# Performance work log

Hardware: AMD Instinct MI355X
Metric: run time of the kernel (lower is better)

## Reference

```python
import jax, jax.numpy as jnp
import numpy as np

N = 100000    # nodes
E = 1600000   # edges (avg degree 16)
IN = 128      # input feature dim
D = 32        # per-head hidden dim
H = 4         # heads for hidden layers
C = 16        # num_classes (final per-head dim)
NEG = 0.2     # leaky_relu negative slope


def setup_inputs() -> dict:
    key = jax.random.key(0)
    ks = jax.random.split(key, 14)
    s = jnp.float32(0.05)
    f32 = jnp.float32
    inp = {
        "inputs": jax.random.normal(ks[0], (N, IN), f32),
        "src": jax.random.randint(ks[1], (E,), 0, N),
        "dst": jax.random.randint(ks[2], (E,), 0, N),
        # layer 0: IN -> (H, D), no residual
        "W0": jax.random.normal(ks[3], (IN, H * D), f32) * s,
        "al0": jax.random.normal(ks[4], (H, D), f32) * s,
        "ar0": jax.random.normal(ks[5], (H, D), f32) * s,
        # layer 1: H*D -> (H, D), identity residual (dims match)
        "W1": jax.random.normal(ks[6], (H * D, H * D), f32) * s,
        "al1": jax.random.normal(ks[7], (H, D), f32) * s,
        "ar1": jax.random.normal(ks[8], (H, D), f32) * s,
        # final layer: H*D -> (1, C), linear residual projection
        "W2": jax.random.normal(ks[9], (H * D, 1 * C), f32) * s,
        "al2": jax.random.normal(ks[10], (1, C), f32) * s,
        "ar2": jax.random.normal(ks[11], (1, C), f32) * s,
        "resW2": jax.random.normal(ks[12], (H * D, 1 * C), f32) * s,
    }
    return inp


def gat_conv(h, W, al, ar, src, dst, n_heads, out_dim, res=None, act=None):
    # h: (N, F_in) -> out: (N, n_heads, out_dim)
    feat = (h @ W).reshape(N, n_heads, out_dim)            # (N,H,D)
    el = jnp.sum(feat * al, axis=-1)                       # (N,H)
    er = jnp.sum(feat * ar, axis=-1)                       # (N,H)
    e = jax.nn.leaky_relu(el[src] + er[dst], NEG)          # (E,H)
    # softmax over incoming edges per destination node
    emax = jax.ops.segment_max(e, dst, num_segments=N)     # (N,H)
    ex = jnp.exp(e - emax[dst])                            # (E,H)
    den = jax.ops.segment_sum(ex, dst, num_segments=N)     # (N,H)
    alpha = ex / den[dst]                                  # (E,H)
    msg = feat[src] * alpha[:, :, None]                    # (E,H,D) -- dominant traffic
    out = jax.ops.segment_sum(msg, dst, num_segments=N)    # (N,H,D)
    if res is not None:
        out = out + res
    if act is not None:
        out = act(out)
    return out


def reference(inputs, src, dst, W0, al0, ar0, W1, al1, ar1, W2, al2, ar2, resW2):
    # hidden layer 0 (no residual), GATConv activation = elu, then flatten + relu
    h = gat_conv(inputs, W0, al0, ar0, src, dst, H, D, res=None, act=jax.nn.elu)
    h = jax.nn.relu(h.reshape(N, H * D))
    # hidden layer 1, identity residual (in == H*D)
    res1 = h.reshape(N, H, D)
    h = gat_conv(h, W1, al1, ar1, src, dst, H, D, res=res1, act=jax.nn.elu)
    h = jax.nn.relu(h.reshape(N, H * D))
    # output layer: 1 head, linear residual projection, no activation, mean over heads
    res2 = (h @ resW2).reshape(N, 1, C)
    out = gat_conv(h, W2, al2, ar2, src, dst, 1, C, res=res2, act=None)
    return out.mean(axis=1)                                # (N, C)
```

## Files before the change

### kernel.cpp

```cpp
#include <hip/hip_runtime.h>

#define N_NODES 100000
#define N_EDGES 1600000
#define IN_F    128
#define NEG_SLOPE 0.2f
#define NBUCK   512
#define BCAP    5120
#define PCHUNK  4096
#define PGRID   391
#define GEMMGRID 1563

typedef __attribute__((ext_vector_type(8))) short bf16x8;
typedef __attribute__((ext_vector_type(4))) float f32x4;

__device__ __forceinline__ float bf2f(unsigned short u) {
    return __uint_as_float(((unsigned int)u) << 16);
}

__device__ __forceinline__ unsigned short f2bf(float f) {
    unsigned int u = __float_as_uint(f);
    u += 0x7FFFu + ((u >> 16) & 1u);
    return (unsigned short)(u >> 16);
}

__global__ __launch_bounds__(256) void init_pack(int* __restrict__ bcursor,
                                                 const float* __restrict__ W0,
                                                 const float* __restrict__ W1,
                                                 const float* __restrict__ W2,
                                                 const float* __restrict__ rW2,
                                                 unsigned short* __restrict__ W0p,
                                                 unsigned short* __restrict__ W1p,
                                                 unsigned short* __restrict__ W2p) {
    const int t = threadIdx.x;
    if (blockIdx.x < 2) {
        int i = blockIdx.x * 256 + t;
        if (i < NBUCK) bcursor[i] = i * BCAP;
        return;
    }
    int gid = (blockIdx.x - 2) * 256 + t;
    const float* W;
    unsigned short* Wp;
    int idx, ncols;
    if (gid < 16384)      { W = W0; Wp = W0p; idx = gid;          ncols = 128; }
    else if (gid < 32768) { W = W1; Wp = W1p; idx = gid - 16384;  ncols = 128; }
    else                  { W = W2; Wp = W2p; idx = gid - 32768;  ncols = 32;  }
    int j  = idx & 7;
    int l  = (idx >> 3) & 63;
    int kt = (idx >> 9) & 3;
    int nt = idx >> 11;
    int k  = kt * 32 + (l >> 4) * 8 + j;
    int n  = nt * 16 + (l & 15);
    float v;
    if (ncols == 128) v = W[k * 128 + n];
    else              v = (n < 16) ? W[k * 16 + n] : rW2[k * 16 + (n - 16)];
    Wp[idx] = f2bf(v);
}

__global__ __launch_bounds__(256) void part_gemm0(const int* __restrict__ src,
                                                  const int* __restrict__ dst,
                                                  int* __restrict__ bcursor,
                                                  unsigned int* __restrict__ pe, int nE,
                                                  const float* __restrict__ A,
                                                  const unsigned short* __restrict__ Wp,
                                                  const float* __restrict__ al,
                                                  const float* __restrict__ ar,
                                                  unsigned short* __restrict__ featb,
                                                  float* __restrict__ el,
                                                  float* __restrict__ er,
                                                  int nrows) {
    __shared__ int hist[NBUCK];
    __shared__ int lstart[NBUCK];
    __shared__ int gbase[NBUCK];
    __shared__ int curB[NBUCK];
    __shared__ int s[NBUCK];
    __shared__ unsigned int reorder[PCHUNK];

    const int t = threadIdx.x;

    if (blockIdx.x < PGRID) {
        const int start = blockIdx.x * PCHUNK;

        hist[t] = 0; hist[t + 256] = 0;
        __syncthreads();
#pragma unroll
        for (int j = 0; j < PCHUNK / 256; ++j) {
            int e = start + j * 256 + t;
            if (e < nE) atomicAdd(&hist[dst[e] >> 8], 1);
        }
        __syncthreads();
        const int c0 = hist[t];
        const int c1 = hist[t + 256];
        s[t] = c0; s[t + 256] = c1;
        __syncthreads();
#pragma unroll
        for (int off = 1; off <= 256; off <<= 1) {
            int x0 = (t >= off) ? s[t - off] : 0;
            int x1 = s[t + 256 - off];
            __syncthreads();
            s[t] += x0; s[t + 256] += x1;
            __syncthreads();
        }
        lstart[t]       = s[t] - c0;
        lstart[t + 256] = s[t + 256] - c1;
        curB[t]         = s[t] - c0;
        curB[t + 256]   = s[t + 256] - c1;
        gbase[t]        = c0 ? atomicAdd(&bcursor[t],       c0) : 0;
        gbase[t + 256]  = c1 ? atomicAdd(&bcursor[t + 256], c1) : 0;
        __syncthreads();

#pragma unroll
        for (int j = 0; j < PCHUNK / 256; ++j) {
            int e = start + j * 256 + t;
            if (e < nE) {
                int d  = dst[e];
                int sv = src[e];
                int b  = d >> 8;
                int pos = atomicAdd(&curB[b], 1);
                reorder[pos] = ((unsigned)sv << 8) | ((unsigned)d & 255u);
            }
        }
        __syncthreads();

        for (int b = t; b < NBUCK; b += 256) {
            int st = lstart[b];
            int en = curB[b];
            int gb = gbase[b];
            for (int k = st; k < en; ++k)
                pe[gb + (k - st)] = reorder[k];
        }
    } else {
        const int bid  = blockIdx.x - PGRID;
        const int wv   = t >> 6;
        const int lane = t & 63;
        const int q    = lane >> 4;
        const int m    = lane & 15;
        const int rb   = bid * 64 + wv * 16;
        const int arow = rb + m;
        const bool rok = arow < nrows;
        const float* Ar = A + (size_t)arow * IN_F;

        f32x4 acc[8];
#pragma unroll
        for (int nt = 0; nt < 8; ++nt) acc[nt] = (f32x4){0.f, 0.f, 0.f, 0.f};

#pragma unroll
        for (int kt = 0; kt < 4; ++kt) {
            bf16x8 afr = (bf16x8){0, 0, 0, 0, 0, 0, 0, 0};
            if (rok) {
                float4 v0 = *(const float4*)(Ar + kt * 32 + q * 8);
                float4 v1 = *(const float4*)(Ar + kt * 32 + q * 8 + 4);
                afr[0] = (short)f2bf(v0.x); afr[1] = (short)f2bf(v0.y);
                afr[2] = (short)f2bf(v0.z); afr[3] = (short)f2bf(v0.w);
                afr[4] = (short)f2bf(v1.x); afr[5] = (short)f2bf(v1.y);
                afr[6] = (short)f2bf(v1.z); afr[7] = (short)f2bf(v1.w);
            }
#pragma unroll
            for (int nt = 0; nt < 8; ++nt) {
                bf16x8 bfr = *(const bf16x8*)(Wp + ((size_t)(nt * 4 + kt) * 64 + lane) * 8);
                acc[nt] = __builtin_amdgcn_mfma_f32_16x16x32_bf16(afr, bfr, acc[nt], 0, 0, 0);
            }
        }

        float pel[16], per[16];
#pragma unroll
        for (int i = 0; i < 16; ++i) { pel[i] = 0.f; per[i] = 0.f; }

#pragma unroll
        for (int nt = 0; nt < 8; ++nt) {
            const int col = nt * 16 + m;
            const float alv = al[col];
            const float arv = ar[col];
            const int h = nt >> 1;
#pragma unroll
            for (int reg = 0; reg < 4; ++reg) {
                int row = rb + q * 4 + reg;
                float a = acc[nt][reg];
                if (row < nrows) featb[(size_t)row * 128 + col] = f2bf(a);
                pel[reg * 4 + h] += a * alv;
                per[reg * 4 + h] += a * arv;
            }
        }
#pragma unroll
        for (int sh = 8; sh > 0; sh >>= 1) {
#pragma unroll
            for (int i = 0; i < 16; ++i) {
                pel[i] += __shfl_down(pel[i], sh);
                per[i] += __shfl_down(per[i], sh);
            }
        }
        if (m == 0) {
#pragma unroll
            for (int reg = 0; reg < 4; ++reg) {
                int row = rb + q * 4 + reg;
                if (row < nrows) {
#pragma unroll
                    for (int h = 0; h < 4; ++h) {
                        el[row * 4 + h] = pel[reg * 4 + h];
                        er[row * 4 + h] = per[reg * 4 + h];
                    }
                }
            }
        }
    }
}

__global__ __launch_bounds__(256) void bucket_finalize(const unsigned int* __restrict__ pe,
                                                       const int* __restrict__ bcursor,
                                                       int* __restrict__ rowptr,
                                                       int* __restrict__ deg,
                                                       int* __restrict__ sorted_src) {
    __shared__ int deg_l[256];
    __shared__ int s[256];
    __shared__ int cur[256];

    const int b  = blockIdx.x;
    const int t  = threadIdx.x;
    const int base = b * BCAP;
    const int cnt  = bcursor[b] - base;
    const int n    = b * 256 + t;

    deg_l[t] = 0;
    __syncthreads();
    for (int i = t; i < cnt; i += 256)
        atomicAdd(&deg_l[pe[base + i] & 255u], 1);
    __syncthreads();

    const int dv = deg_l[t];
    s[t] = dv;
    __syncthreads();
#pragma unroll
    for (int off = 1; off < 256; off <<= 1) {
        int x = (t >= off) ? s[t - off] : 0;
        __syncthreads();
        s[t] += x;
        __syncthreads();
    }
    const int off_l = s[t] - dv;
    if (n < N_NODES) {
        rowptr[n] = base + off_l;
        deg[n]    = dv;
    }
    cur[t] = off_l;
    __syncthreads();

    for (int i = t; i < cnt; i += 256) {
        unsigned int ed = pe[base + i];
        int pos = atomicAdd(&cur[ed & 255u], 1);
        sorted_src[base + pos] = (int)(ed >> 8);
    }
}

__global__ __launch_bounds__(256) void gemm128_mfma_bf16(const unsigned short* __restrict__ Ab,
                                                         const unsigned short* __restrict__ Wp,
                                                         const float* __restrict__ al,
                                                         const float* __restrict__ ar,
                                                         unsigned short* __restrict__ featb,
                                                         float* __restrict__ el,
                                                         float* __restrict__ er,
                                                         int nrows) {
    const int t    = threadIdx.x;
    const int wv   = t >> 6;
    const int lane = t & 63;
    const int q    = lane >> 4;
    const int m    = lane & 15;
    const int rb   = blockIdx.x * 64 + wv * 16;
    const int arow = rb + m;
    const bool rok = arow < nrows;
    const unsigned short* Ar = Ab + (size_t)arow * IN_F;

    f32x4 acc[8];
#pragma unroll
    for (int nt = 0; nt < 8; ++nt) acc[nt] = (f32x4){0.f, 0.f, 0.f, 0.f};

#pragma unroll
    for (int kt = 0; kt < 4; ++kt) {
        bf16x8 afr = (bf16x8){0, 0, 0, 0, 0, 0, 0, 0};
        if (rok) afr = *(const bf16x8*)(Ar + kt * 32 + q * 8);
#pragma unroll
        for (int nt = 0; nt < 8; ++nt) {
            bf16x8 bfr = *(const bf16x8*)(Wp + ((size_t)(nt * 4 + kt) * 64 + lane) * 8);
            acc[nt] = __builtin_amdgcn_mfma_f32_16x16x32_bf16(afr, bfr, acc[nt], 0, 0, 0);
        }
    }

    float pel[16], per[16];
#pragma unroll
    for (int i = 0; i < 16; ++i) { pel[i] = 0.f; per[i] = 0.f; }

#pragma unroll
    for (int nt = 0; nt < 8; ++nt) {
        const int col = nt * 16 + m;
        const float alv = al[col];
        const float arv = ar[col];
        const int h = nt >> 1;
#pragma unroll
        for (int reg = 0; reg < 4; ++reg) {
            int row = rb + q * 4 + reg;
            float a = acc[nt][reg];
            if (row < nrows) featb[(size_t)row * 128 + col] = f2bf(a);
            pel[reg * 4 + h] += a * alv;
            per[reg * 4 + h] += a * arv;
        }
    }
#pragma unroll
    for (int sh = 8; sh > 0; sh >>= 1) {
#pragma unroll
        for (int i = 0; i < 16; ++i) {
            pel[i] += __shfl_down(pel[i], sh);
            per[i] += __shfl_down(per[i], sh);
        }
    }
    if (m == 0) {
#pragma unroll
        for (int reg = 0; reg < 4; ++reg) {
            int row = rb + q * 4 + reg;
            if (row < nrows) {
#pragma unroll
                for (int h = 0; h < 4; ++h) {
                    el[row * 4 + h] = pel[reg * 4 + h];
                    er[row * 4 + h] = per[reg * 4 + h];
                }
            }
        }
    }
}

__global__ __launch_bounds__(256) void gemm16_mfma(const unsigned short* __restrict__ Ab,
                                                   const unsigned short* __restrict__ Wp,
                                                   const float* __restrict__ al,
                                                   const float* __restrict__ ar,
                                                   unsigned short* __restrict__ feat2b,
                                                   float* __restrict__ res2,
                                                   float* __restrict__ el,
                                                   float* __restrict__ er,
                                                   int nrows) {
    const int t    = threadIdx.x;
    const int wv   = t >> 6;
    const int lane = t & 63;
    const int q    = lane >> 4;
    const int m    = lane & 15;
    const int rb   = blockIdx.x * 64 + wv * 16;
    const int arow = rb + m;
    const bool rok = arow < nrows;
    const unsigned short* Ar = Ab + (size_t)arow * IN_F;

    f32x4 acc0 = (f32x4){0.f, 0.f, 0.f, 0.f};
    f32x4 acc1 = (f32x4){0.f, 0.f, 0.f, 0.f};

#pragma unroll
    for (int kt = 0; kt < 4; ++kt) {
        bf16x8 afr = (bf16x8){0, 0, 0, 0, 0, 0, 0, 0};
        if (rok) afr = *(const bf16x8*)(Ar + kt * 32 + q * 8);
        bf16x8 b0 = *(const bf16x8*)(Wp + ((size_t)(0 * 4 + kt) * 64 + lane) * 8);
        bf16x8 b1 = *(const bf16x8*)(Wp + ((size_t)(1 * 4 + kt) * 64 + lane) * 8);
        acc0 = __builtin_amdgcn_mfma_f32_16x16x32_bf16(afr, b0, acc0, 0, 0, 0);
        acc1 = __builtin_amdgcn_mfma_f32_16x16x32_bf16(afr, b1, acc1, 0, 0, 0);
    }

    float pel[4], per[4];
    const float alv = al[m];
    const float arv = ar[m];
#pragma unroll
    for (int reg = 0; reg < 4; ++reg) {
        int row = rb + q * 4 + reg;
        float a = acc0[reg];
        if (row < nrows) {
            feat2b[(size_t)row * 16 + m] = f2bf(a);
            res2[(size_t)row * 16 + m]   = acc1[reg];
        }
        pel[reg] = a * alv;
        per[reg] = a * arv;
    }
#pragma unroll
    for (int sh = 8; sh > 0; sh >>= 1) {
#pragma unroll
        for (int reg = 0; reg < 4; ++reg) {
            pel[reg] += __shfl_down(pel[reg], sh);
            per[reg] += __shfl_down(per[reg], sh);
        }
    }
    if (m == 0) {
#pragma unroll
        for (int reg = 0; reg < 4; ++reg) {
            int row = rb + q * 4 + reg;
            if (row < nrows) { el[row] = pel[reg]; er[row] = per[reg]; }
        }
    }
}

#define LOAD16(B, START, CNT)                                                  \
    {                                                                          \
        _Pragma("unroll")                                                      \
        for (int jg_ = 0; jg_ < 16; jg_ += 4) {                                \
            if (jg_ < (CNT)) {                                                 \
                _Pragma("unroll")                                              \
                for (int k_ = 0; k_ < 4; ++k_) {                               \
                    int sj_ = __builtin_amdgcn_readlane(s_own, (START) + jg_ + k_); \
                    const unsigned short* rp_ = featb + (size_t)sj_ * 128;     \
                    (B)[jg_ + k_] = *((const ushort2*)rp_ + lane);             \
                }                                                              \
            }                                                                  \
        }                                                                      \
    }

__global__ __launch_bounds__(256) void gat_agg128(const int* __restrict__ rowptr,
                                                  const int* __restrict__ deg,
                                                  const int* __restrict__ sorted_src,
                                                  const float* __restrict__ el,
                                                  const float* __restrict__ er,
                                                  const unsigned short* __restrict__ featb,
                                                  const unsigned short* __restrict__ resb,
                                                  unsigned short* __restrict__ outb) {
    __shared__ float sW[4][64][4];

    const int wv   = threadIdx.x >> 6;
    const int lane = threadIdx.x & 63;
    const int nd   = blockIdx.x * 4 + wv;

    const int dg = deg[nd];
    const int r0 = rowptr[nd];
    const int h  = lane >> 4;
    const float4 er4 = *(const float4*)(er + nd * 4);

    float den = 0.f;
    float ax = 0.f, ay = 0.f;

    for (int base = 0; base < dg; base += 64) {
        int m = dg - base; if (m > 64) m = 64;

        int s_own = 0;
        if (lane < m) s_own = sorted_src[r0 + base + lane];

        ushort2 u[16], v[16];
        int c = m < 16 ? m : 16;
        LOAD16(u, 0, c)

        float4 w4;
        if (lane < m) {
            float4 e4 = *(const float4*)(el + s_own * 4);
            float t_;
            t_ = e4.x + er4.x; t_ = t_ > 0.f ? t_ : NEG_SLOPE * t_; w4.x = __expf(t_);
            t_ = e4.y + er4.y; t_ = t_ > 0.f ? t_ : NEG_SLOPE * t_; w4.y = __expf(t_);
            t_ = e4.z + er4.z; t_ = t_ > 0.f ? t_ : NEG_SLOPE * t_; w4.z = __expf(t_);
            t_ = e4.w + er4.w; t_ = t_ > 0.f ? t_ : NEG_SLOPE * t_; w4.w = __expf(t_);
        } else {
            w4.x = 0.f; w4.y = 0.f; w4.z = 0.f; w4.w = 0.f;
        }
        *(float4*)(&sW[wv][lane][0]) = w4;

        int i = 0;
        while (true) {
            int in_ = i + c;
            int cn = m - in_; if (cn > 16) cn = 16;
            if (cn > 0) LOAD16(v, in_, cn)

            const float* wb = &sW[wv][i][h];
#pragma unroll
            for (int jg = 0; jg < 16; jg += 4) {
                if (jg < c) {
#pragma unroll
                    for (int k = 0; k < 4; ++k) {
                        float w = wb[(jg + k) * 4];
                        ushort2 uu = u[jg + k];
                        den += w;
                        ax += w * bf2f(uu.x);
                        ay += w * bf2f(uu.y);
                    }
                }
            }
            if (cn <= 0) break;
#pragma unroll
            for (int k = 0; k < 16; ++k) u[k] = v[k];
            i = in_; c = cn;
        }
    }

    float scale = den > 0.f ? 1.f / den : 0.f;
    float ox = ax * scale, oy = ay * scale;
    size_t o0 = (size_t)nd * 128 + lane * 2;
    if (resb) {
        ushort2 rv = *(const ushort2*)(resb + o0);
        ox += bf2f(rv.x);
        oy += bf2f(rv.y);
    }
    ox = fmaxf(ox, 0.f);
    oy = fmaxf(oy, 0.f);
    ushort2 ou;
    ou.x = f2bf(ox);
    ou.y = f2bf(oy);
    *(ushort2*)(outb + o0) = ou;
}

__global__ __launch_bounds__(256) void gat_agg16(const int* __restrict__ rowptr,
                                                 const int* __restrict__ deg,
                                                 const int* __restrict__ sorted_src,
                                                 const float* __restrict__ el,
                                                 const float* __restrict__ er,
                                                 const unsigned short* __restrict__ feat2b,
                                                 const float* __restrict__ res,
                                                 float* __restrict__ out) {
    __shared__ int   sS[4][64];
    __shared__ float sW[4][64];

    const int wv   = threadIdx.x >> 6;
    const int lane = threadIdx.x & 63;
    const int nd   = blockIdx.x * 4 + (threadIdx.x >> 6);
    const int g    = lane >> 3;
    const int f2   = (lane & 7) * 2;

    const int dg = deg[nd];
    const int r0 = rowptr[nd];
    const float erd = er[nd];

    float ax = 0.f, ay = 0.f, den = 0.f;

    for (int base = 0; base < dg; base += 64) {
        int m = dg - base; if (m > 64) m = 64;
        if (lane < m) {
            int s = sorted_src[r0 + base + lane];
            sS[wv][lane] = s;
            float v = el[s] + erd;
            v = v > 0.f ? v : NEG_SLOPE * v;
            sW[wv][lane] = __expf(v);
        }
        for (int i = g; i < m; i += 8) {
            int s   = sS[wv][i];
            float w = sW[wv][i];
            den += w;
            ushort2 u = *(const ushort2*)(feat2b + (size_t)s * 16 + f2);
            ax += w * bf2f(u.x);
            ay += w * bf2f(u.y);
        }
    }

    ax += __shfl_down(ax, 32); ay += __shfl_down(ay, 32); den += __shfl_down(den, 32);
    ax += __shfl_down(ax, 16); ay += __shfl_down(ay, 16); den += __shfl_down(den, 16);
    ax += __shfl_down(ax, 8);  ay += __shfl_down(ay, 8);  den += __shfl_down(den, 8);

    if (lane < 8) {
        float scale = den > 0.f ? 1.f / den : 0.f;
        size_t o0 = (size_t)nd * 16 + f2;
        float2 o;
        o.x = ax * scale + res[o0];
        o.y = ay * scale + res[o0 + 1];
        *(float2*)(out + o0) = o;
    }
}

extern "C" void kernel_launch(void* const* d_in, const int* in_sizes, int n_in,
                              void* d_out, int out_size, void* d_ws, size_t ws_size,
                              hipStream_t stream) {
    const float* inputs = (const float*)d_in[0];
    const int*   src    = (const int*)d_in[1];
    const int*   dst    = (const int*)d_in[2];
    const float* W0     = (const float*)d_in[3];
    const float* al0    = (const float*)d_in[4];
    const float* ar0    = (const float*)d_in[5];
    const float* W1     = (const float*)d_in[6];
    const float* al1    = (const float*)d_in[7];
    const float* ar1    = (const float*)d_in[8];
    const float* W2     = (const float*)d_in[9];
    const float* al2    = (const float*)d_in[10];
    const float* ar2    = (const float*)d_in[11];
    const float* resW2  = (const float*)d_in[12];
    float* out = (float*)d_out;

    const size_t NF = (size_t)N_NODES * 128;
    float* ws   = (float*)d_ws;
    float* el   = ws;
    float* er   = el + (size_t)N_NODES * 4;
    float* res2 = er + (size_t)N_NODES * 4;
    unsigned short* hbufb  = (unsigned short*)(res2 + (size_t)N_NODES * 16);
    unsigned short* featb  = hbufb + NF;
    unsigned short* feat2b = featb + NF;
    unsigned short* W0p    = feat2b + (size_t)N_NODES * 16;
    unsigned short* W1p    = W0p + 16384;
    unsigned short* W2p    = W1p + 16384;
    int* iws = (int*)(W2p + 8192);
    unsigned int* pe = (unsigned int*)iws;
    int* sorted_src  = iws + NBUCK * BCAP;
    int* deg         = sorted_src + NBUCK * BCAP;
    int* rowptr      = deg + N_NODES;
    int* bcursor     = rowptr + N_NODES;

    dim3 blk(256);
    int aggGrid = N_NODES / 4;

    init_pack<<<162, blk, 0, stream>>>(bcursor, W0, W1, W2, resW2, W0p, W1p, W2p);
    part_gemm0<<<PGRID + GEMMGRID, blk, 0, stream>>>(src, dst, bcursor, pe, N_EDGES,
                                                     inputs, W0p, al0, ar0, featb,
                                                     el, er, N_NODES);
    bucket_finalize<<<PGRID, blk, 0, stream>>>(pe, bcursor, rowptr, deg, sorted_src);

    gat_agg128<<<aggGrid, blk, 0, stream>>>(rowptr, deg, sorted_src, el, er, featb,
                                            nullptr, hbufb);

    gemm128_mfma_bf16<<<GEMMGRID, blk, 0, stream>>>(hbufb, W1p, al1, ar1, featb,
                                                    el, er, N_NODES);
    gat_agg128<<<aggGrid, blk, 0, stream>>>(rowptr, deg, sorted_src, el, er, featb,
                                            hbufb, hbufb);

    gemm16_mfma<<<GEMMGRID, blk, 0, stream>>>(hbufb, W2p, al2, ar2, feat2b, res2,
                                              el, er, N_NODES);
    gat_agg16<<<aggGrid, blk, 0, stream>>>(rowptr, deg, sorted_src, el, er, feat2b,
                                           res2, out);
}
```

Before: 392.1 us.

## Store pre-scaled byte offsets and stage edges in LDS for 8-wide gathers

Bucket finalize now stores src*256 as a byte offset instead of the source index. The aggregation kernels shift that offset to address el and the feature rows directly, which removes 64-bit index multiplies. gat_agg128 replaces the readlane/double-buffer register scheme with LDS staging of offsets and per-head weights, issuing 8 independent 32-bit gathers per iteration. The softmax denominator becomes per-lane partial sums reduced once at the end by shuffle. This cuts address arithmetic and the serial per-edge den accumulation, at the cost of LDS traffic and padding to multiples of 8 (padded slots use offset 0 with weight 0, so extra loads hit valid memory).

```diff
diff --git a/kernel.cpp b/kernel.cpp
--- a/kernel.cpp
+++ b/kernel.cpp
@@ -21,6 +21,10 @@
     unsigned int u = __float_as_uint(f);
     u += 0x7FFFu + ((u >> 16) & 1u);
     return (unsigned short)(u >> 16);
+}
+
+__device__ __forceinline__ unsigned int ld_u32(const char* base, unsigned int off) {
+    return *(const unsigned int*)(base + off);
 }
 
 __global__ __launch_bounds__(256) void init_pack(int* __restrict__ bcursor,
@@ -208,7 +212,7 @@
                                                        const int* __restrict__ bcursor,
                                                        int* __restrict__ rowptr,
                                                        int* __restrict__ deg,
-                                                       int* __restrict__ sorted_src) {
+                                                       int* __restrict__ sorted_boff) {
     __shared__ int deg_l[256];
     __shared__ int s[256];
     __shared__ int cur[256];
@@ -246,7 +250,7 @@
     for (int i = t; i < cnt; i += 256) {
         unsigned int ed = pe[base + i];
         int pos = atomicAdd(&cur[ed & 255u], 1);
-        sorted_src[base + pos] = (int)(ed >> 8);
+        sorted_boff[base + pos] = (int)(ed & 0xFFFFFF00u);
     }
 }
 
@@ -388,30 +392,16 @@
     }
 }
 
-#define LOAD16(B, START, CNT)                                                  \
-    {                                                                          \
-        _Pragma("unroll")                                                      \
-        for (int jg_ = 0; jg_ < 16; jg_ += 4) {                                \
-            if (jg_ < (CNT)) {                                                 \
-                _Pragma("unroll")                                              \
-                for (int k_ = 0; k_ < 4; ++k_) {                               \
-                    int sj_ = __builtin_amdgcn_readlane(s_own, (START) + jg_ + k_); \
-                    const unsigned short* rp_ = featb + (size_t)sj_ * 128;     \
-                    (B)[jg_ + k_] = *((const ushort2*)rp_ + lane);             \
-                }                                                              \
-            }                                                                  \
-        }                                                                      \
-    }
-
 __global__ __launch_bounds__(256) void gat_agg128(const int* __restrict__ rowptr,
                                                   const int* __restrict__ deg,
-                                                  const int* __restrict__ sorted_src,
+                                                  const int* __restrict__ sorted_boff,
                                                   const float* __restrict__ el,
                                                   const float* __restrict__ er,
                                                   const unsigned short* __restrict__ featb,
                                                   const unsigned short* __restrict__ resb,
                                                   unsigned short* __restrict__ outb) {
-    __shared__ float sW[4][64][4];
+    __shared__ __align__(16) int   sS[4][64];
+    __shared__ __align__(16) float sW[4][4][68];
 
     const int wv   = threadIdx.x >> 6;
     const int lane = threadIdx.x & 63;
@@ -420,60 +410,78 @@
     const int dg = deg[nd];
     const int r0 = rowptr[nd];
     const int h  = lane >> 4;
+    const unsigned int lane4 = (unsigned int)(lane << 2);
     const float4 er4 = *(const float4*)(er + nd * 4);
-
-    float den = 0.f;
+    const char* fb = (const char*)featb;
+    const char* eb = (const char*)el;
+
+    float dx = 0.f, dy = 0.f, dz = 0.f, dw = 0.f;
     float ax = 0.f, ay = 0.f;
 
     for (int base = 0; base < dg; base += 64) {
         int m = dg - base; if (m > 64) m = 64;
 
-        int s_own = 0;
-        if (lane < m) s_own = sorted_src[r0 + base + lane];
-
-        ushort2 u[16], v[16];
-        int c = m < 16 ? m : 16;
-        LOAD16(u, 0, c)
-
-        float4 w4;
+        int boff = 0;
+        float4 w4 = {0.f, 0.f, 0.f, 0.f};
         if (lane < m) {
-            float4 e4 = *(const float4*)(el + s_own * 4);
+            boff = sorted_boff[r0 + base + lane];
+            float4 e4 = *(const float4*)(eb + (unsigned int)(boff >> 4));
             float t_;
             t_ = e4.x + er4.x; t_ = t_ > 0.f ? t_ : NEG_SLOPE * t_; w4.x = __expf(t_);
             t_ = e4.y + er4.y; t_ = t_ > 0.f ? t_ : NEG_SLOPE * t_; w4.y = __expf(t_);
             t_ = e4.z + er4.z; t_ = t_ > 0.f ? t_ : NEG_SLOPE * t_; w4.z = __expf(t_);
             t_ = e4.w + er4.w; t_ = t_ > 0.f ? t_ : NEG_SLOPE * t_; w4.w = __expf(t_);
-        } else {
-            w4.x = 0.f; w4.y = 0.f; w4.z = 0.f; w4.w = 0.f;
-        }
-        *(float4*)(&sW[wv][lane][0]) = w4;
-
-        int i = 0;
-        while (true) {
-            int in_ = i + c;
-            int cn = m - in_; if (cn > 16) cn = 16;
-            if (cn > 0) LOAD16(v, in_, cn)
-
-            const float* wb = &sW[wv][i][h];
-#pragma unroll
-            for (int jg = 0; jg < 16; jg += 4) {
-                if (jg < c) {
-#pragma unroll
-                    for (int k = 0; k < 4; ++k) {
-                        float w = wb[(jg + k) * 4];
-                        ushort2 uu = u[jg + k];
-                        den += w;
-                        ax += w * bf2f(uu.x);
-                        ay += w * bf2f(uu.y);
-                    }
-                }
-            }
-            if (cn <= 0) break;
-#pragma unroll
-            for (int k = 0; k < 16; ++k) u[k] = v[k];
-            i = in_; c = cn;
-        }
-    }
+        }
+        sS[wv][lane]    = boff;
+        sW[wv][0][lane] = w4.x;
+        sW[wv][1][lane] = w4.y;
+        sW[wv][2][lane] = w4.z;
+        sW[wv][3][lane] = w4.w;
+        dx += w4.x; dy += w4.y; dz += w4.z; dw += w4.w;
+
+        const int mr = (m + 7) & ~7;
+        for (int i = 0; i < mr; i += 8) {
+            const int4   sa = *(const int4*)(&sS[wv][i]);
+            const int4   sb = *(const int4*)(&sS[wv][i + 4]);
+            const float4 wa = *(const float4*)(&sW[wv][h][i]);
+            const float4 wb = *(const float4*)(&sW[wv][h][i + 4]);
+
+            unsigned int u0 = ld_u32(fb, (unsigned int)sa.x + lane4);
+            unsigned int u1 = ld_u32(fb, (unsigned int)sa.y + lane4);
+            unsigned int u2 = ld_u32(fb, (unsigned int)sa.z + lane4);
+            unsigned int u3 = ld_u32(fb, (unsigned int)sa.w + lane4);
+            unsigned int u4 = ld_u32(fb, (unsigned int)sb.x + lane4);
+            unsigned int u5 = ld_u32(fb, (unsigned int)sb.y + lane4);
+            unsigned int u6 = ld_u32(fb, (unsigned int)sb.z + lane4);
+            unsigned int u7 = ld_u32(fb, (unsigned int)sb.w + lane4);
+
+            ax += wa.x * __uint_as_float(u0 << 16);
+            ay += wa.x * __uint_as_float(u0 & 0xFFFF0000u);
+            ax += wa.y * __uint_as_float(u1 << 16);
+            ay += wa.y * __uint_as_float(u1 & 0xFFFF0000u);
+            ax += wa.z * __uint_as_float(u2 << 16);
+            ay += wa.z * __uint_as_float(u2 & 0xFFFF0000u);
+            ax += wa.w * __uint_as_float(u3 << 16);
+            ay += wa.w * __uint_as_float(u3 & 0xFFFF0000u);
+            ax += wb.x * __uint_as_float(u4 << 16);
+            ay += wb.x * __uint_as_float(u4 & 0xFFFF0000u);
+            ax += wb.y * __uint_as_float(u5 << 16);
+            ay += wb.y * __uint_as_float(u5 & 0xFFFF0000u);
+            ax += wb.z * __uint_as_float(u6 << 16);
+            ay += wb.z * __uint_as_float(u6 & 0xFFFF0000u);
+            ax += wb.w * __uint_as_float(u7 << 16);
+            ay += wb.w * __uint_as_float(u7 & 0xFFFF0000u);
+        }
+    }
+
+#pragma unroll
+    for (int sh = 1; sh < 64; sh <<= 1) {
+        dx += __shfl_xor(dx, sh);
+        dy += __shfl_xor(dy, sh);
+        dz += __shfl_xor(dz, sh);
+        dw += __shfl_xor(dw, sh);
+    }
+    float den = (h == 0) ? dx : (h == 1) ? dy : (h == 2) ? dz : dw;
 
     float scale = den > 0.f ? 1.f / den : 0.f;
     float ox = ax * scale, oy = ay * scale;
@@ -493,7 +501,7 @@
 
 __global__ __launch_bounds__(256) void gat_agg16(const int* __restrict__ rowptr,
                                                  const int* __restrict__ deg,
-                                                 const int* __restrict__ sorted_src,
+                                                 const int* __restrict__ sorted_boff,
                                                  const float* __restrict__ el,
                                                  const float* __restrict__ er,
                                                  const unsigned short* __restrict__ feat2b,
@@ -506,7 +514,9 @@
     const int lane = threadIdx.x & 63;
     const int nd   = blockIdx.x * 4 + (threadIdx.x >> 6);
     const int g    = lane >> 3;
-    const int f2   = (lane & 7) * 2;
+    const unsigned int flane4 = (unsigned int)((lane & 7) << 2);
+    const char* f2base = (const char*)feat2b;
+    const char* eb = (const char*)el;
 
     const int dg = deg[nd];
     const int r0 = rowptr[nd];
@@ -517,19 +527,19 @@
     for (int base = 0; base < dg; base += 64) {
         int m = dg - base; if (m > 64) m = 64;
         if (lane < m) {
-            int s = sorted_src[r0 + base + lane];
-            sS[wv][lane] = s;
-            float v = el[s] + erd;
+            int boff = sorted_boff[r0 + base + lane];
+            sS[wv][lane] = boff;
+            float v = *(const float*)(eb + (unsigned int)(boff >> 6)) + erd;
             v = v > 0.f ? v : NEG_SLOPE * v;
             sW[wv][lane] = __expf(v);
         }
         for (int i = g; i < m; i += 8) {
-            int s   = sS[wv][i];
+            int bo  = sS[wv][i];
             float w = sW[wv][i];
             den += w;
-            ushort2 u = *(const ushort2*)(feat2b + (size_t)s * 16 + f2);
-            ax += w * bf2f(u.x);
-            ay += w * bf2f(u.y);
+            unsigned int u = *(const unsigned int*)(f2base + (unsigned int)(bo >> 3) + flane4);
+            ax += w * __uint_as_float(u << 16);
+            ay += w * __uint_as_float(u & 0xFFFF0000u);
         }
     }
 
@@ -539,7 +549,7 @@
 
     if (lane < 8) {
         float scale = den > 0.f ? 1.f / den : 0.f;
-        size_t o0 = (size_t)nd * 16 + f2;
+        size_t o0 = (size_t)nd * 16 + ((lane & 7) << 1);
         float2 o;
         o.x = ax * scale + res[o0];
         o.y = ay * scale + res[o0 + 1];
@@ -578,8 +588,8 @@
     unsigned short* W2p    = W1p + 16384;
     int* iws = (int*)(W2p + 8192);
     unsigned int* pe = (unsigned int*)iws;
-    int* sorted_src  = iws + NBUCK * BCAP;
-    int* deg         = sorted_src + NBUCK * BCAP;
+    int* sorted_boff = iws + NBUCK * BCAP;
+    int* deg         = sorted_boff + NBUCK * BCAP;
     int* rowptr      = deg + N_NODES;
     int* bcursor     = rowptr + N_NODES;
 
@@ -590,18 +600,18 @@
     part_gemm0<<<PGRID + GEMMGRID, blk, 0, stream>>>(src, dst, bcursor, pe, N_EDGES,
                                                      inputs, W0p, al0, ar0, featb,
                                                      el, er, N_NODES);
-    bucket_finalize<<<PGRID, blk, 0, stream>>>(pe, bcursor, rowptr, deg, sorted_src);
-
-    gat_agg128<<<aggGrid, blk, 0, stream>>>(rowptr, deg, sorted_src, el, er, featb,
+    bucket_finalize<<<PGRID, blk, 0, stream>>>(pe, bcursor, rowptr, deg, sorted_boff);
+
+    gat_agg128<<<aggGrid, blk, 0, stream>>>(rowptr, deg, sorted_boff, el, er, featb,
                                             nullptr, hbufb);
 
     gemm128_mfma_bf16<<<GEMMGRID, blk, 0, stream>>>(hbufb, W1p, al1, ar1, featb,
                                                     el, er, N_NODES);
-    gat_agg128<<<aggGrid, blk, 0, stream>>>(rowptr, deg, sorted_src, el, er, featb,
+    gat_agg128<<<aggGrid, blk, 0, stream>>>(rowptr, deg, sorted_boff, el, er, featb,
                                             hbufb, hbufb);
 
     gemm16_mfma<<<GEMMGRID, blk, 0, stream>>>(hbufb, W2p, al2, ar2, feat2b, res2,
                                               el, er, N_NODES);
-    gat_agg16<<<aggGrid, blk, 0, stream>>>(rowptr, deg, sorted_src, el, er, feat2b,
+    gat_agg16<<<aggGrid, blk, 0, stream>>>(rowptr, deg, sorted_boff, el, er, feat2b,
                                            res2, out);
 }
```

Result: faster. 377.4 us, median of 2 (-3.8%).
